# Kernel optimization log

Hardware: AMD Instinct MI355X
Metric: run time of the kernel (lower is better)

Reference implementation:

```python
import jax, jax.numpy as jnp
import numpy as np

NW, NT = 200000, 100000
DW, DT = 128, 64
HID, HEADS, OUT = 64, 2, 2
HC = HID * HEADS  # 128
E = 500000
NEG_SLOPE = 0.2


def setup_inputs() -> dict:
    key = jax.random.key(0)
    ks = iter(jax.random.split(key, 40))

    def nrm(shape, scale):
        return jax.random.normal(next(ks), shape, dtype=jnp.float32) * scale

    inp = {
        "x_wallet": nrm((NW, DW), 1.0),
        "x_token": nrm((NT, DT), 1.0),
        # per-node-type input projections Linear(in, hidden)
        "lin_w_W": nrm((DW, HID), 1.0 / np.sqrt(DW)),
        "lin_w_b": jnp.zeros((HID,), jnp.float32),
        "lin_t_W": nrm((DT, HID), 1.0 / np.sqrt(DT)),
        "lin_t_b": jnp.zeros((HID,), jnp.float32),
        # GAT layer 0: in=HID(64) -> H*C(128), stacked over 3 edge types
        "Wsrc0": nrm((3, HID, HC), 1.0 / np.sqrt(HID)),
        "Wdst0": nrm((3, HID, HC), 1.0 / np.sqrt(HID)),
        "atts0": nrm((3, HEADS, HID), 1.0 / np.sqrt(HID)),
        "attd0": nrm((3, HEADS, HID), 1.0 / np.sqrt(HID)),
        "b0": jnp.zeros((3, HC), jnp.float32),
        # GAT layer 1: in=H*C(128) -> H*C(128)
        "Wsrc1": nrm((3, HC, HC), 1.0 / np.sqrt(HC)),
        "Wdst1": nrm((3, HC, HC), 1.0 / np.sqrt(HC)),
        "atts1": nrm((3, HEADS, HID), 1.0 / np.sqrt(HID)),
        "attd1": nrm((3, HEADS, HID), 1.0 / np.sqrt(HID)),
        "b1": jnp.zeros((3, HC), jnp.float32),
        # classifiers Linear(H*C, out)
        "cls_w_W": nrm((HC, OUT), 1.0 / np.sqrt(HC)),
        "cls_w_b": jnp.zeros((OUT,), jnp.float32),
        "cls_t_W": nrm((HC, OUT), 1.0 / np.sqrt(HC)),
        "cls_t_b": jnp.zeros((OUT,), jnp.float32),
        # edge indices: [2, E] with row0 = src ids, row1 = dst ids
        "e_wt": jnp.stack([jax.random.randint(next(ks), (E,), 0, NW),
                            jax.random.randint(next(ks), (E,), 0, NT)]).astype(jnp.int64),
        "e_tw": jnp.stack([jax.random.randint(next(ks), (E,), 0, NT),
                            jax.random.randint(next(ks), (E,), 0, NW)]).astype(jnp.int64),
        "e_ww": jnp.stack([jax.random.randint(next(ks), (E,), 0, NW),
                            jax.random.randint(next(ks), (E,), 0, NW)]).astype(jnp.int64),
    }
    return inp


def gat_conv(x_src, x_dst, edge, Wsrc, Wdst, att_s, att_d, bias, n_dst):
    # bipartite GATConv: project, per-edge attention, segment softmax over dst, scatter-sum
    hs = (x_src @ Wsrc).reshape(-1, HEADS, HID)  # [Ns,H,C]
    hd = (x_dst @ Wdst).reshape(-1, HEADS, HID)  # [Nd,H,C]
    a_s = jnp.einsum("nhc,hc->nh", hs, att_s)    # [Ns,H]
    a_d = jnp.einsum("nhc,hc->nh", hd, att_d)    # [Nd,H]
    s, d = edge[0], edge[1]
    alpha = jax.nn.leaky_relu(a_s[s] + a_d[d], NEG_SLOPE)  # [E,H]
    m = jax.ops.segment_max(alpha, d, num_segments=n_dst)
    m = jnp.where(jnp.isfinite(m), m, 0.0)  # nodes with no in-edges
    ex = jnp.exp(alpha - m[d])
    den = jax.ops.segment_sum(ex, d, num_segments=n_dst)
    alpha = ex / (den[d] + 1e-16)
    out = jax.ops.segment_sum(alpha[:, :, None] * hs[s], d, num_segments=n_dst)  # [Nd,H,C]
    return out.reshape(n_dst, HC) + bias


def reference(x_wallet, x_token, lin_w_W, lin_w_b, lin_t_W, lin_t_b,
              Wsrc0, Wdst0, atts0, attd0, b0,
              Wsrc1, Wdst1, atts1, attd1, b1,
              cls_w_W, cls_w_b, cls_t_W, cls_t_b,
              e_wt, e_tw, e_ww):
    xw = x_wallet @ lin_w_W + lin_w_b
    xt = x_token @ lin_t_W + lin_t_b
    for Wsrc, Wdst, ats, atd, b in ((Wsrc0, Wdst0, atts0, attd0, b0),
                                     (Wsrc1, Wdst1, atts1, attd1, b1)):
        # edge type 0: wallet->token, 1: token->wallet, 2: wallet->wallet; HeteroConv aggr='sum'
        out_t = gat_conv(xw, xt, e_wt, Wsrc[0], Wdst[0], ats[0], atd[0], b[0], NT)
        out_w = (gat_conv(xt, xw, e_tw, Wsrc[1], Wdst[1], ats[1], atd[1], b[1], NW)
                 + gat_conv(xw, xw, e_ww, Wsrc[2], Wdst[2], ats[2], atd[2], b[2], NW))
        xw = jax.nn.elu(out_w)
        xt = jax.nn.elu(out_t)
    logits_w = xw @ cls_w_W + cls_w_b  # [NW,2]
    logits_t = xt @ cls_t_W + cls_t_b  # [NT,2]
    return jnp.concatenate([logits_w, logits_t], axis=0)  # [NW+NT,2]
```

## Files before the change

### kernel.cpp

```cpp
#include <hip/hip_runtime.h>
#include <stdint.h>

typedef unsigned short ushort_t;
typedef short s8v __attribute__((ext_vector_type(8)));
typedef float f4v __attribute__((ext_vector_type(4)));

#define NW 200000
#define NT 100000
#define EE 500000
#define NSEG (NT + NW + NW)

constexpr int HGRID = 1536;
constexpr int FGRID = 1536;
constexpr int AWG   = (NW + 255) / 256;
constexpr int ATG   = (NT + 255) / 256;
constexpr int TGRID = NT / 4;
constexpr int WGRID = NW / 4;

__device__ __forceinline__ float b2f(unsigned short u){
  union { unsigned int i; float f; } v; v.i = ((unsigned int)u) << 16; return v.f;
}
__device__ __forceinline__ unsigned short f2b(float f){
  unsigned int x = __float_as_uint(f);
  unsigned int r = x + 0x7fffu + ((x >> 16) & 1u);
  return (unsigned short)(r >> 16);
}
__device__ __forceinline__ float ldf(const void* p, long idx, int fm){
  return fm ? ((const float*)p)[idx] : b2f(((const ushort_t*)p)[idx]);
}

__global__ void detect_kern(const int* ewt, const int* etw, const int* eww,
                            const unsigned* xw_words, int* mode){
  if (threadIdx.x == 0 && blockIdx.x == 0){
    unsigned o = 0;
    for (int i = 0; i < 64; ++i)
      o |= (unsigned)ewt[2 * i + 1] | (unsigned)etw[2 * i + 1] | (unsigned)eww[2 * i + 1];
    mode[0] = (o == 0) ? 1 : 0;
    int viol = 0;
    for (int i = 0; i < 256; ++i){
      unsigned s = xw_words[i] & 0xffffu;
      unsigned e = (s >> 7) & 0xffu;
      if (!(s == 0u || s == 0x8000u || (e >= 90u && e <= 140u))) viol++;
    }
    mode[1] = (viol > 8) ? 1 : 0;
  }
}

struct TDesc { const void* src; ushort_t* dst; long ebase; int K; int N; };
struct TDesc8 { TDesc d[8]; };
__device__ __forceinline__ void transpose_body(const TDesc8& td, int fm, int b){
  int mi = b >> 6;
  TDesc t = td.d[mi];
  int e = ((b & 63) << 8) + threadIdx.x;
  if (e < t.K * t.N){
    int k = e / t.N, n = e - k * t.N;
    t.dst[n * t.K + k] = f2b(ldf(t.src, t.ebase + e, fm));
  }
}

__device__ __forceinline__ void uprep_body(const void* Wsrc0, const void* Wdst0, const void* atts0,
    const void* attd0, const void* Wsrc1, const void* Wdst1, const void* atts1, const void* attd1,
    float* Uw0, float* Ut0, float* Uw1, float* Ut1, int fm, int id){
  if (id >= (64 + 128) * 12) return;
  int layer = (id >= 64 * 12);
  int rem = layer ? id - 64 * 12 : id;
  int K = layer ? 128 : 64;
  int k = rem / 12, j = rem % 12;
  const void* Ws = layer ? Wsrc1 : Wsrc0;
  const void* Wd = layer ? Wdst1 : Wdst0;
  const void* As = layer ? atts1 : atts0;
  const void* Ad = layer ? attd1 : attd0;
  int t, h; bool src;
  if (j < 8){ const int tt[8] = {0,0,2,2,1,1,2,2}; t = tt[j]; h = j & 1; src = (j < 4); }
  else { int jj = j - 8; t = (jj < 2) ? 1 : 0; h = jj & 1; src = (jj < 2); }
  const void* W = src ? Ws : Wd;
  const void* A = src ? As : Ad;
  float acc = 0.f;
  for (int c = 0; c < 64; ++c)
    acc += ldf(W, (long)(t * K + k) * 128 + h * 64 + c, fm) * ldf(A, t * 128 + h * 64 + c, fm);
  if (j < 8) (layer ? Uw1 : Uw0)[k * 8 + j] = acc;
  else       (layer ? Ut1 : Ut0)[k * 4 + (j - 8)] = acc;
}

__device__ __forceinline__ void hist_loop(const int* ewt, const int* etw, const int* eww,
    int md, int* deg, int b, int nb){
  int t0 = b * 256 + (int)threadIdx.x;
  int step = nb * 256;
  for (int i = t0; i < 3 * EE; i += step){
    int t = i / EE, e = i - t * EE;
    const int* ep = (t == 0) ? ewt : (t == 1) ? etw : eww;
    int d = md ? ep[2 * (EE + e)] : ep[EE + e];
    int base = (t == 0) ? 0 : (t == 1) ? NT : NT + NW;
    atomicAdd(&deg[base + d], 1);
  }
}

__device__ __forceinline__ void fill_loop(const int* ewt, const int* etw, const int* eww,
    int md, int* cursor, int* adj, int b, int nb){
  int t0 = b * 256 + (int)threadIdx.x;
  int step = nb * 256;
  for (int i = t0; i < 3 * EE; i += step){
    int t = i / EE, e = i - t * EE;
    const int* ep = (t == 0) ? ewt : (t == 1) ? etw : eww;
    int s = md ? ep[2 * e] : ep[e];
    int d = md ? ep[2 * (EE + e)] : ep[EE + e];
    int base = (t == 0) ? 0 : (t == 1) ? NT : NT + NW;
    int pos = atomicAdd(&cursor[base + d], 1);
    adj[pos] = s;
  }
}

__global__ __launch_bounds__(512) void scan1(const int* deg, int* excl, int* sums){
  __shared__ int pair[512];
  int t = threadIdx.x;
  int base = blockIdx.x * 1024;
  int i0 = base + 2 * t;
  int a = (i0 < NSEG) ? deg[i0] : 0;
  int b = (i0 + 1 < NSEG) ? deg[i0 + 1] : 0;
  int ps = a + b;
  pair[t] = ps;
  __syncthreads();
  for (int off = 1; off < 512; off <<= 1){
    int v = (t >= off) ? pair[t - off] : 0;
    __syncthreads();
    if (t >= off) pair[t] += v;
    __syncthreads();
  }
  int epair = pair[t] - ps;
  if (i0 < NSEG) excl[i0] = epair;
  if (i0 + 1 < NSEG) excl[i0 + 1] = epair + a;
  if (t == 511) sums[blockIdx.x] = pair[511];
}

__global__ __launch_bounds__(512) void scan2(int* sums, int nch){
  __shared__ int s[512];
  int t = threadIdx.x;
  int orig = (t < nch) ? sums[t] : 0;
  s[t] = orig;
  __syncthreads();
  for (int off = 1; off < 512; off <<= 1){
    int v = (t >= off) ? s[t - off] : 0;
    __syncthreads();
    if (t >= off) s[t] += v;
    __syncthreads();
  }
  if (t < nch) sums[t] = s[t] - orig;
}

__global__ void scan3(int* rowptr, int* cursor, const int* sums){
  int i = blockIdx.x * 256 + threadIdx.x;
  if (i < NSEG){
    int v = rowptr[i] + sums[i >> 10];
    rowptr[i] = v; cursor[i] = v;
  }
  if (i == 0) rowptr[NSEG] = 3 * EE;
}

template<int K, int NC, int RS, bool BIAS, bool EXTA>
__device__ __forceinline__ void gemm_body(const void* __restrict__ A, const ushort_t* __restrict__ Bt,
    const void* __restrict__ bias, ushort_t* __restrict__ C, int M, int fm, int nchunk,
    int bid, int gstr){
  constexpr int CT = NC / 16, KK = K / 32;
  int tid = threadIdx.x, lane = tid & 63, wave = tid >> 6;
  int rl = lane & 15, kq = (lane >> 4) * 8;
  s8v bfrag[CT][KK];
#pragma unroll
  for (int ct = 0; ct < CT; ++ct)
#pragma unroll
    for (int kk = 0; kk < KK; ++kk)
      bfrag[ct][kk] = *(const s8v*)(Bt + (long)(ct * 16 + rl) * K + kk * 32 + kq);
  float biasv[CT];
  if (BIAS){
#pragma unroll
    for (int ct = 0; ct < CT; ++ct) biasv[ct] = ldf(bias, ct * 16 + rl, fm);
  }
  for (int chunk = bid; chunk < nchunk; chunk += gstr){
    long m0 = (long)chunk * 128 + wave * 32;
    f4v acc[2][CT];
#pragma unroll
    for (int rt = 0; rt < 2; ++rt)
#pragma unroll
      for (int ct = 0; ct < CT; ++ct) acc[rt][ct] = (f4v){0.f, 0.f, 0.f, 0.f};
#pragma unroll
    for (int rt = 0; rt < 2; ++rt){
      long row = m0 + rt * 16 + rl;
      bool ok = row < (long)M;
#pragma unroll
      for (int kk = 0; kk < KK; ++kk){
        s8v a = (s8v){0,0,0,0,0,0,0,0};
        if (ok){
          long e = row * K + kk * 32 + kq;
          if (EXTA && fm){
            const float* p = (const float*)A + e;
            uint4 lo = *(const uint4*)p;
            uint4 hi = *(const uint4*)(p + 4);
            union { s8v v; unsigned u[4]; } t;
            t.u[0] = (unsigned)f2b(__uint_as_float(lo.x)) | ((unsigned)f2b(__uint_as_float(lo.y)) << 16);
            t.u[1] = (unsigned)f2b(__uint_as_float(lo.z)) | ((unsigned)f2b(__uint_as_float(lo.w)) << 16);
            t.u[2] = (unsigned)f2b(__uint_as_float(hi.x)) | ((unsigned)f2b(__uint_as_float(hi.y)) << 16);
            t.u[3] = (unsigned)f2b(__uint_as_float(hi.z)) | ((unsigned)f2b(__uint_as_float(hi.w)) << 16);
            a = t.v;
          } else {
            a = *(const s8v*)((const ushort_t*)A + e);
          }
        }
#pragma unroll
        for (int ct = 0; ct < CT; ++ct)
          acc[rt][ct] = __builtin_amdgcn_mfma_f32_16x16x32_bf16(a, bfrag[ct][kk], acc[rt][ct], 0, 0, 0);
      }
    }
#pragma unroll
    for (int rt = 0; rt < 2; ++rt){
      long rbase = (long)chunk * 128 + wave * 32 + rt * 16 + (lane >> 4) * 4;
#pragma unroll
      for (int ct = 0; ct < CT; ++ct){
#pragma unroll
        for (int r = 0; r < 4; ++r){
          long gm = rbase + r;
          if (gm < (long)M){
            float v = acc[rt][ct][r];
            if (BIAS) v += biasv[ct];
            C[gm * RS + ct * 16 + rl] = f2b(v);
          }
        }
      }
    }
  }
}

template<int K, bool WAL>
__device__ __forceinline__ void a_body(const ushort_t* __restrict__ x, const float* __restrict__ U,
    float* __restrict__ dpq, float* __restrict__ spqA, float* __restrict__ spqB, int N, int n){
  constexpr int NCOL = WAL ? 8 : 4;
  if (n >= N) return;
  float acc[NCOL];
#pragma unroll
  for (int j = 0; j < NCOL; ++j) acc[j] = 0.f;
  const ushort_t* xr = x + (long)n * K;
#pragma unroll
  for (int k8 = 0; k8 < K / 8; ++k8){
    uint4 v = *(const uint4*)(xr + k8 * 8);
    unsigned uu[4] = {v.x, v.y, v.z, v.w};
#pragma unroll
    for (int i = 0; i < 4; ++i){
      float f0 = b2f((unsigned short)(uu[i] & 0xffffu));
      float f1 = b2f((unsigned short)(uu[i] >> 16));
      const float* Ur = U + (k8 * 8 + i * 2) * NCOL;
#pragma unroll
      for (int j = 0; j < NCOL; ++j) acc[j] += f0 * Ur[j] + f1 * Ur[NCOL + j];
    }
  }
  if (WAL){
    f4v tA = {__expf(acc[0]), __expf(0.2f * acc[0]), __expf(acc[1]), __expf(0.2f * acc[1])};
    *(f4v*)(spqA + (long)n * 4) = tA;
    f4v tB = {__expf(acc[2]), __expf(0.2f * acc[2]), __expf(acc[3]), __expf(0.2f * acc[3])};
    *(f4v*)(spqB + (long)n * 4) = tB;
    f4v d1 = {__expf(acc[4]), __expf(0.2f * acc[4]), __expf(acc[5]), __expf(0.2f * acc[5])};
    f4v d2 = {__expf(acc[6]), __expf(0.2f * acc[6]), __expf(acc[7]), __expf(0.2f * acc[7])};
    *(f4v*)(dpq + (long)n * 8) = d1;
    *(f4v*)(dpq + (long)n * 8 + 4) = d2;
  } else {
    f4v tA = {__expf(acc[0]), __expf(0.2f * acc[0]), __expf(acc[1]), __expf(0.2f * acc[1])};
    *(f4v*)(spqA + (long)n * 4) = tA;
    f4v d0 = {__expf(acc[2]), __expf(0.2f * acc[2]), __expf(acc[3]), __expf(0.2f * acc[3])};
    *(f4v*)(dpq + (long)n * 4) = d0;
  }
}

__device__ __forceinline__ void round_load(const int* __restrict__ adj, int j, int cnt,
    const ushort_t* __restrict__ hs, const float* __restrict__ spq, int c0, int hh,
    float2 (&pq)[8], unsigned (&h)[8]){
#pragma unroll
  for (int i = 0; i < 8; ++i){
    if (i < cnt){
      int s = adj[j + i];
      pq[i] = *(const float2*)(spq + s * 4 + hh * 2);
      h[i] = *(const unsigned*)(hs + (long)s * 128 + c0);
    }
  }
}

__device__ __forceinline__ void round_acc(int cnt, float pd, float qd,
    const float2 (&pq)[8], const unsigned (&h)[8], float& n0, float& n1, float& den){
#pragma unroll
  for (int i = 0; i < 8; ++i){
    if (i < cnt){
      float t = pq[i].x * pd, u = pq[i].y * qd;
      float w = t > 1.f ? t : u;
      den += w;
      n0 += w * b2f((unsigned short)(h[i] & 0xffffu));
      n1 += w * b2f((unsigned short)(h[i] >> 16));
    }
  }
}

__device__ __forceinline__ void classify_store(float o0, float o1, const void* W, const void* b,
    int lane, long g, void* dout, int fm){
  float w00 = ldf(W, 4 * lane + 0, fm), w01 = ldf(W, 4 * lane + 1, fm);
  float w10 = ldf(W, 4 * lane + 2, fm), w11 = ldf(W, 4 * lane + 3, fm);
  float p0 = o0 * w00 + o1 * w10;
  float p1 = o0 * w01 + o1 * w11;
#pragma unroll
  for (int off = 32; off > 0; off >>= 1){ p0 += __shfl_xor(p0, off, 64); p1 += __shfl_xor(p1, off, 64); }
  if (lane == 0){
    float r0 = p0 + ldf(b, 0, fm);
    float r1 = p1 + ldf(b, 1, fm);
    if (fm){ ((float*)dout)[g * 2] = r0; ((float*)dout)[g * 2 + 1] = r1; }
    else { ((ushort_t*)dout)[g * 2] = f2b(r0); ((ushort_t*)dout)[g * 2 + 1] = f2b(r1); }
  }
}

template<bool FINAL>
__device__ __forceinline__ void agg_tok_body(const int* __restrict__ rowptr, const int* __restrict__ adj,
    const float* __restrict__ atd, const float* __restrict__ spq0, const ushort_t* __restrict__ hs0,
    const void* __restrict__ bsrc, ushort_t* __restrict__ xt_out,
    const void* __restrict__ clsWt, const void* __restrict__ clsbt,
    void* __restrict__ dout, int fm, int db){
  int wv = __builtin_amdgcn_readfirstlane(threadIdx.x >> 6);
  int lane = threadIdx.x & 63;
  int hh = lane >> 5, c0 = lane << 1;
  int d = db * 4 + wv;
  float2 dq = *(const float2*)(atd + (long)d * 4 + hh * 2);
  int beg = rowptr[d], end = rowptr[d + 1];
  float n0 = 0.f, n1 = 0.f, den = 0.f;
  for (int j = beg; j < end; j += 8){
    int cnt = min(end - j, 8);
    float2 pq[8]; unsigned h[8];
    round_load(adj, j, cnt, hs0, spq0, c0, hh, pq, h);
    round_acc(cnt, dq.x, dq.y, pq, h, n0, n1, den);
  }
  float inv = 1.f / (den + 1e-16f);
  float o0 = n0 * inv + ldf(bsrc, c0, fm);
  float o1 = n1 * inv + ldf(bsrc, c0 + 1, fm);
  o0 = o0 > 0.f ? o0 : __expf(o0) - 1.f;
  o1 = o1 > 0.f ? o1 : __expf(o1) - 1.f;
  if (!FINAL){
    unsigned pack = (unsigned)f2b(o0) | ((unsigned)f2b(o1) << 16);
    *(unsigned*)(xt_out + (long)d * 128 + c0) = pack;
  } else {
    classify_store(o0, o1, clsWt, clsbt, lane, (long)NW + d, dout, fm);
  }
}

template<bool FINAL>
__global__ __launch_bounds__(256) void agg_wal(const int* __restrict__ rowptr, const int* __restrict__ adj,
    const float* __restrict__ awd, const float* __restrict__ spq1, const float* __restrict__ spq2,
    const ushort_t* __restrict__ hs1, const ushort_t* __restrict__ hs2,
    const void* __restrict__ bsrc, ushort_t* __restrict__ xw_out,
    const void* __restrict__ clsWw, const void* __restrict__ clsbw,
    void* __restrict__ dout, const int* __restrict__ mode){
  int fm = mode[1];
  int wv = __builtin_amdgcn_readfirstlane(threadIdx.x >> 6);
  int lane = threadIdx.x & 63;
  int hh = lane >> 5, c0 = lane << 1;
  int d = blockIdx.x * 4 + wv;
  float2 dq1 = *(const float2*)(awd + (long)d * 8 + hh * 2);
  float2 dq2 = *(const float2*)(awd + (long)d * 8 + 4 + hh * 2);
  int s1 = NT + d, s2 = NT + NW + d;
  int b1 = rowptr[s1], e1 = rowptr[s1 + 1];
  int b2 = rowptr[s2], e2 = rowptr[s2 + 1];
  int c1 = min(e1 - b1, 8), c2 = min(e2 - b2, 8);
  float n10 = 0.f, n11 = 0.f, den1 = 0.f;
  float n20 = 0.f, n21 = 0.f, den2 = 0.f;
  {
    float2 pq1[8], pq2[8]; unsigned h1[8], h2[8];
    if (c1 > 0) round_load(adj, b1, c1, hs1, spq1, c0, hh, pq1, h1);
    if (c2 > 0) round_load(adj, b2, c2, hs2, spq2, c0, hh, pq2, h2);
    if (c1 > 0) round_acc(c1, dq1.x, dq1.y, pq1, h1, n10, n11, den1);
    if (c2 > 0) round_acc(c2, dq2.x, dq2.y, pq2, h2, n20, n21, den2);
  }
  for (int j = b1 + 8; j < e1; j += 8){
    int cnt = min(e1 - j, 8);
    float2 pq[8]; unsigned h[8];
    round_load(adj, j, cnt, hs1, spq1, c0, hh, pq, h);
    round_acc(cnt, dq1.x, dq1.y, pq, h, n10, n11, den1);
  }
  for (int j = b2 + 8; j < e2; j += 8){
    int cnt = min(e2 - j, 8);
    float2 pq[8]; unsigned h[8];
    round_load(adj, j, cnt, hs2, spq2, c0, hh, pq, h);
    round_acc(cnt, dq2.x, dq2.y, pq, h, n20, n21, den2);
  }
  float i1v = 1.f / (den1 + 1e-16f), i2v = 1.f / (den2 + 1e-16f);
  float o0 = n10 * i1v + n20 * i2v + ldf(bsrc, 128 + c0, fm)     + ldf(bsrc, 256 + c0, fm);
  float o1 = n11 * i1v + n21 * i2v + ldf(bsrc, 128 + c0 + 1, fm) + ldf(bsrc, 256 + c0 + 1, fm);
  o0 = o0 > 0.f ? o0 : __expf(o0) - 1.f;
  o1 = o1 > 0.f ? o1 : __expf(o1) - 1.f;
  if (!FINAL){
    unsigned pack = (unsigned)f2b(o0) | ((unsigned)f2b(o1) << 16);
    *(unsigned*)(xw_out + (long)d * 128 + c0) = pack;
  } else {
    classify_store(o0, o1, clsWw, clsbw, lane, (long)d, dout, fm);
  }
}


__global__ __launch_bounds__(256) void k_tu(TDesc8 td,
    const void* Wsrc0, const void* Wdst0, const void* atts0, const void* attd0,
    const void* Wsrc1, const void* Wdst1, const void* atts1, const void* attd1,
    float* Uw0, float* Ut0, float* Uw1, float* Ut1, const int* mode){
  int b = blockIdx.x, fm = mode[1];
  if (b < 512){ transpose_body(td, fm, b); return; }
  uprep_body(Wsrc0, Wdst0, atts0, attd0, Wsrc1, Wdst1, atts1, attd1,
             Uw0, Ut0, Uw1, Ut1, fm, (b - 512) * 256 + (int)threadIdx.x);
}

__global__ __launch_bounds__(256, 2) void k_pre(
    const void* xw_in, const ushort_t* BtLw, const void* lwb, ushort_t* xw0,
    const void* xt_in, const ushort_t* BtLt, const void* ltb, ushort_t* xt0,
    const int* ewt, const int* etw, const int* eww, int* deg,
    const int* mode, int ncW, int ncT){
  int b = blockIdx.x;
  if (b < 512){ gemm_body<128, 64, 64, true, true>(xw_in, BtLw, lwb, xw0, NW, mode[1], ncW, b, 512); return; }
  b -= 512;
  if (b < 256){ gemm_body<64, 64, 64, true, true>(xt_in, BtLt, ltb, xt0, NT, mode[1], ncT, b, 256); return; }
  b -= 256;
  hist_loop(ewt, etw, eww, mode[0], deg, b, HGRID);
}

__global__ __launch_bounds__(256, 2) void k_fill(
    const ushort_t* xw0, const ushort_t* xt0, const ushort_t* BtS0w, ushort_t* hs0,
    const float* Uw0, const float* Ut0, float* awd, float* atd,
    float* spq0, float* spq1, float* spq2,
    const int* ewt, const int* etw, const int* eww, int* cursor, int* adj,
    const int* mode, int ncW){
  int b = blockIdx.x;
  if (b < 512){ gemm_body<64, 128, 128, false, false>(xw0, BtS0w, nullptr, hs0, NW, 0, ncW, b, 512); return; }
  b -= 512;
  if (b < FGRID){ fill_loop(ewt, etw, eww, mode[0], cursor, adj, b, FGRID); return; }
  b -= FGRID;
  if (b < AWG){ a_body<64, true>(xw0, Uw0, awd, spq0, spq2, NW, b * 256 + (int)threadIdx.x); return; }
  b -= AWG;
  a_body<64, false>(xt0, Ut0, atd, spq1, nullptr, NT, b * 256 + (int)threadIdx.x);
}

__global__ __launch_bounds__(256, 2) void k_tok0(
    const ushort_t* xt0, const ushort_t* xw0, const ushort_t* BtS0t, const ushort_t* BtS0w2,
    ushort_t* hs1, ushort_t* hs2,
    const int* rowptr, const int* adj, const float* atd, const float* spq0,
    const ushort_t* hs0, const void* b0, ushort_t* xtB,
    const int* mode, int ncT, int ncW){
  int b = blockIdx.x;
  if (b < 256){ gemm_body<64, 128, 128, false, false>(xt0, BtS0t, nullptr, hs1, NT, 0, ncT, b, 256); return; }
  b -= 256;
  if (b < 384){ gemm_body<64, 128, 128, false, false>(xw0, BtS0w2, nullptr, hs2, NW, 0, ncW, b, 384); return; }
  b -= 384;
  agg_tok_body<false>(rowptr, adj, atd, spq0, hs0, b0, xtB, nullptr, nullptr, nullptr, mode[1], b);
}

__global__ __launch_bounds__(256, 2) void k_mid1(
    const ushort_t* xwB, const ushort_t* xtB, const ushort_t* BtS1w, ushort_t* hs0,
    const float* Uw1, const float* Ut1, float* awd, float* atd,
    float* spq0, float* spq1, float* spq2, const int* mode, int ncW){
  int b = blockIdx.x;
  if (b < 512){ gemm_body<128, 128, 128, false, false>(xwB, BtS1w, nullptr, hs0, NW, 0, ncW, b, 512); return; }
  b -= 512;
  if (b < AWG){ a_body<128, true>(xwB, Uw1, awd, spq0, spq2, NW, b * 256 + (int)threadIdx.x); return; }
  b -= AWG;
  a_body<128, false>(xtB, Ut1, atd, spq1, nullptr, NT, b * 256 + (int)threadIdx.x);
}

__global__ __launch_bounds__(256, 2) void k_fin1(
    const ushort_t* xtB, const ushort_t* xwB, const ushort_t* BtS1t, const ushort_t* BtS1w2,
    ushort_t* hs1, ushort_t* hs2,
    const int* rowptr, const int* adj, const float* atd, const float* spq0,
    const ushort_t* hs0, const void* b1, const void* clsWt, const void* clsbt,
    void* dout, const int* mode, int ncT, int ncW){
  int b = blockIdx.x;
  if (b < 256){ gemm_body<128, 128, 128, false, false>(xtB, BtS1t, nullptr, hs1, NT, 0, ncT, b, 256); return; }
  b -= 256;
  if (b < 384){ gemm_body<128, 128, 128, false, false>(xwB, BtS1w2, nullptr, hs2, NW, 0, ncW, b, 384); return; }
  b -= 384;
  agg_tok_body<true>(rowptr, adj, atd, spq0, hs0, b1, nullptr, clsWt, clsbt, dout, mode[1], b);
}

extern "C" void kernel_launch(void* const* d_in, const int* in_sizes, int n_in,
                              void* d_out, int out_size, void* d_ws, size_t ws_size,
                              hipStream_t stream){
  const void* x_wallet = d_in[0];
  const void* x_token  = d_in[1];
  const void* lin_w_W  = d_in[2];
  const void* lin_w_b  = d_in[3];
  const void* lin_t_W  = d_in[4];
  const void* lin_t_b  = d_in[5];
  const void* Wsrc0    = d_in[6];
  const void* Wdst0    = d_in[7];
  const void* atts0    = d_in[8];
  const void* attd0    = d_in[9];
  const void* b0       = d_in[10];
  const void* Wsrc1    = d_in[11];
  const void* Wdst1    = d_in[12];
  const void* atts1    = d_in[13];
  const void* attd1    = d_in[14];
  const void* b1       = d_in[15];
  const void* cls_w_W  = d_in[16];
  const void* cls_w_b  = d_in[17];
  const void* cls_t_W  = d_in[18];
  const void* cls_t_b  = d_in[19];
  const int* e_wt = (const int*)d_in[20];
  const int* e_tw = (const int*)d_in[21];
  const int* e_ww = (const int*)d_in[22];

  char* ws = (char*)d_ws;
  size_t off = 0;
  auto alloc = [&](size_t bytes) -> char* {
    char* p = ws + off; off += (bytes + 255) & ~(size_t)255; return p;
  };
  int* rowptr = (int*)alloc((size_t)(NSEG + 1) * 4);
  int* deg    = (int*)alloc((size_t)(NSEG + 1) * 4);
  int* adj    = (int*)alloc((size_t)3 * EE * 4);
  int* sums   = (int*)alloc(512 * 4);
  int* mode   = (int*)alloc(8);
  ushort_t* BtLw = (ushort_t*)alloc(64 * 128 * 2);
  ushort_t* BtLt = (ushort_t*)alloc(64 * 64 * 2);
  ushort_t* BtS0 = (ushort_t*)alloc(3 * 128 * 64 * 2);
  ushort_t* BtS1 = (ushort_t*)alloc(3 * 128 * 128 * 2);
  float* Uw0 = (float*)alloc(64 * 8 * 4);
  float* Ut0 = (float*)alloc(64 * 4 * 4);
  float* Uw1 = (float*)alloc(128 * 8 * 4);
  float* Ut1 = (float*)alloc(128 * 4 * 4);
  float* awd = (float*)alloc((size_t)NW * 8 * 4);
  float* atd = (float*)alloc((size_t)NT * 4 * 4);
  float* spq0 = (float*)alloc((size_t)NW * 4 * 4);
  float* spq1 = (float*)alloc((size_t)NT * 4 * 4);
  float* spq2 = (float*)alloc((size_t)NW * 4 * 4);
  ushort_t* hs0 = (ushort_t*)alloc((size_t)NW * 128 * 2);
  ushort_t* hs1 = (ushort_t*)alloc((size_t)NT * 128 * 2);
  ushort_t* hs2 = (ushort_t*)alloc((size_t)NW * 128 * 2);
  ushort_t* xbuf = (ushort_t*)alloc(((size_t)NW + NT) * 128 * 2);
  ushort_t* xw0 = xbuf;
  ushort_t* xt0 = xbuf + (size_t)NW * 64;
  ushort_t* xwB = xbuf;
  ushort_t* xtB = xbuf + (size_t)NW * 128;
  (void)in_sizes; (void)n_in;

  if (off > ws_size){
    hipMemsetAsync(d_out, 0, (size_t)out_size * 2, stream);
    return;
  }

  hipMemsetAsync(deg, 0, (size_t)NSEG * 4, stream);
  detect_kern<<<1, 64, 0, stream>>>(e_wt, e_tw, e_ww, (const unsigned*)x_wallet, mode);

  TDesc8 td;
  td.d[0] = { lin_w_W, BtLw, 0, 128, 64 };
  td.d[1] = { lin_t_W, BtLt, 0, 64, 64 };
  for (int t = 0; t < 3; ++t){
    td.d[2 + t] = { Wsrc0, BtS0 + t * 128 * 64,  (long)t * 64 * 128,  64,  128 };
    td.d[5 + t] = { Wsrc1, BtS1 + t * 128 * 128, (long)t * 128 * 128, 128, 128 };
  }
  int ncW = (NW + 127) / 128, ncT = (NT + 127) / 128;

  k_tu<<<521, 256, 0, stream>>>(td, Wsrc0, Wdst0, atts0, attd0, Wsrc1, Wdst1, atts1, attd1,
                                Uw0, Ut0, Uw1, Ut1, mode);
  k_pre<<<512 + 256 + HGRID, 256, 0, stream>>>(x_wallet, BtLw, lin_w_b, xw0,
                                               x_token, BtLt, lin_t_b, xt0,
                                               e_wt, e_tw, e_ww, deg, mode, ncW, ncT);
  int nch = (NSEG + 1023) / 1024;
  scan1<<<nch, 512, 0, stream>>>(deg, rowptr, sums);
  scan2<<<1, 512, 0, stream>>>(sums, nch);
  scan3<<<(NSEG + 255) / 256, 256, 0, stream>>>(rowptr, deg, sums);

  k_fill<<<512 + FGRID + AWG + ATG, 256, 0, stream>>>(xw0, xt0, BtS0, hs0,
      Uw0, Ut0, awd, atd, spq0, spq1, spq2, e_wt, e_tw, e_ww, deg, adj, mode, ncW);
  k_tok0<<<256 + 384 + TGRID, 256, 0, stream>>>(xt0, xw0, BtS0 + 128 * 64, BtS0 + 2 * 128 * 64,
      hs1, hs2, rowptr, adj, atd, spq0, hs0, b0, xtB, mode, ncT, ncW);
  agg_wal<false><<<WGRID, 256, 0, stream>>>(rowptr, adj, awd, spq1, spq2, hs1, hs2, b0, xwB,
                                            nullptr, nullptr, nullptr, mode);

  k_mid1<<<512 + AWG + ATG, 256, 0, stream>>>(xwB, xtB, BtS1, hs0,
      Uw1, Ut1, awd, atd, spq0, spq1, spq2, mode, ncW);
  k_fin1<<<256 + 384 + TGRID, 256, 0, stream>>>(xtB, xwB, BtS1 + 128 * 128, BtS1 + 2 * 128 * 128,
      hs1, hs2, rowptr, adj, atd, spq0, hs0, b1, cls_t_W, cls_t_b, d_out, mode, ncT, ncW);
  agg_wal<true><<<WGRID, 256, 0, stream>>>(rowptr, adj, awd, spq1, spq2, hs1, hs2, b1, nullptr,
                                           cls_w_W, cls_w_b, d_out, mode);
}
```

Measured before the change: 906.8 us.

## Regroup GEMMs into one fused launch and split token aggregation into own kernel

All three source-projection GEMMs for each layer now run in a single fused launch alongside edge fill and attention-score work. Token aggregation becomes its own standalone kernel without the occupancy-2 launch bound. Previously it shared a launch with two GEMMs. The aim is to give the aggregation its own register and occupancy budget and to pack the GEMM work more evenly. The cost is that the GEMMs no longer overlap with the token gather.

```diff
diff --git a/kernel.cpp b/kernel.cpp
--- a/kernel.cpp
+++ b/kernel.cpp
@@ -311,15 +311,16 @@
 }
 
 template<bool FINAL>
-__device__ __forceinline__ void agg_tok_body(const int* __restrict__ rowptr, const int* __restrict__ adj,
+__global__ __launch_bounds__(256) void agg_tok(const int* __restrict__ rowptr, const int* __restrict__ adj,
     const float* __restrict__ atd, const float* __restrict__ spq0, const ushort_t* __restrict__ hs0,
     const void* __restrict__ bsrc, ushort_t* __restrict__ xt_out,
     const void* __restrict__ clsWt, const void* __restrict__ clsbt,
-    void* __restrict__ dout, int fm, int db){
+    void* __restrict__ dout, const int* __restrict__ mode){
+  int fm = mode[1];
   int wv = __builtin_amdgcn_readfirstlane(threadIdx.x >> 6);
   int lane = threadIdx.x & 63;
   int hh = lane >> 5, c0 = lane << 1;
-  int d = db * 4 + wv;
+  int d = blockIdx.x * 4 + wv;
   float2 dq = *(const float2*)(atd + (long)d * 4 + hh * 2);
   int beg = rowptr[d], end = rowptr[d + 1];
   float n0 = 0.f, n1 = 0.f, den = 0.f;
@@ -418,15 +419,21 @@
   hist_loop(ewt, etw, eww, mode[0], deg, b, HGRID);
 }
 
-__global__ __launch_bounds__(256, 2) void k_fill(
-    const ushort_t* xw0, const ushort_t* xt0, const ushort_t* BtS0w, ushort_t* hs0,
+__global__ __launch_bounds__(256, 2) void k_gemms0(
+    const ushort_t* xw0, const ushort_t* xt0,
+    const ushort_t* BtS0w, const ushort_t* BtS0t, const ushort_t* BtS0w2,
+    ushort_t* hs0, ushort_t* hs1, ushort_t* hs2,
     const float* Uw0, const float* Ut0, float* awd, float* atd,
     float* spq0, float* spq1, float* spq2,
     const int* ewt, const int* etw, const int* eww, int* cursor, int* adj,
-    const int* mode, int ncW){
+    const int* mode, int ncW, int ncT){
   int b = blockIdx.x;
   if (b < 512){ gemm_body<64, 128, 128, false, false>(xw0, BtS0w, nullptr, hs0, NW, 0, ncW, b, 512); return; }
   b -= 512;
+  if (b < 256){ gemm_body<64, 128, 128, false, false>(xt0, BtS0t, nullptr, hs1, NT, 0, ncT, b, 256); return; }
+  b -= 256;
+  if (b < 384){ gemm_body<64, 128, 128, false, false>(xw0, BtS0w2, nullptr, hs2, NW, 0, ncW, b, 384); return; }
+  b -= 384;
   if (b < FGRID){ fill_loop(ewt, etw, eww, mode[0], cursor, adj, b, FGRID); return; }
   b -= FGRID;
   if (b < AWG){ a_body<64, true>(xw0, Uw0, awd, spq0, spq2, NW, b * 256 + (int)threadIdx.x); return; }
@@ -434,44 +441,22 @@
   a_body<64, false>(xt0, Ut0, atd, spq1, nullptr, NT, b * 256 + (int)threadIdx.x);
 }
 
-__global__ __launch_bounds__(256, 2) void k_tok0(
-    const ushort_t* xt0, const ushort_t* xw0, const ushort_t* BtS0t, const ushort_t* BtS0w2,
-    ushort_t* hs1, ushort_t* hs2,
-    const int* rowptr, const int* adj, const float* atd, const float* spq0,
-    const ushort_t* hs0, const void* b0, ushort_t* xtB,
-    const int* mode, int ncT, int ncW){
-  int b = blockIdx.x;
-  if (b < 256){ gemm_body<64, 128, 128, false, false>(xt0, BtS0t, nullptr, hs1, NT, 0, ncT, b, 256); return; }
-  b -= 256;
-  if (b < 384){ gemm_body<64, 128, 128, false, false>(xw0, BtS0w2, nullptr, hs2, NW, 0, ncW, b, 384); return; }
-  b -= 384;
-  agg_tok_body<false>(rowptr, adj, atd, spq0, hs0, b0, xtB, nullptr, nullptr, nullptr, mode[1], b);
-}
-
-__global__ __launch_bounds__(256, 2) void k_mid1(
-    const ushort_t* xwB, const ushort_t* xtB, const ushort_t* BtS1w, ushort_t* hs0,
+__global__ __launch_bounds__(256, 2) void k_gemms1(
+    const ushort_t* xwB, const ushort_t* xtB,
+    const ushort_t* BtS1w, const ushort_t* BtS1t, const ushort_t* BtS1w2,
+    ushort_t* hs0, ushort_t* hs1, ushort_t* hs2,
     const float* Uw1, const float* Ut1, float* awd, float* atd,
-    float* spq0, float* spq1, float* spq2, const int* mode, int ncW){
+    float* spq0, float* spq1, float* spq2, const int* mode, int ncW, int ncT){
   int b = blockIdx.x;
   if (b < 512){ gemm_body<128, 128, 128, false, false>(xwB, BtS1w, nullptr, hs0, NW, 0, ncW, b, 512); return; }
   b -= 512;
-  if (b < AWG){ a_body<128, true>(xwB, Uw1, awd, spq0, spq2, NW, b * 256 + (int)threadIdx.x); return; }
-  b -= AWG;
-  a_body<128, false>(xtB, Ut1, atd, spq1, nullptr, NT, b * 256 + (int)threadIdx.x);
-}
-
-__global__ __launch_bounds__(256, 2) void k_fin1(
-    const ushort_t* xtB, const ushort_t* xwB, const ushort_t* BtS1t, const ushort_t* BtS1w2,
-    ushort_t* hs1, ushort_t* hs2,
-    const int* rowptr, const int* adj, const float* atd, const float* spq0,
-    const ushort_t* hs0, const void* b1, const void* clsWt, const void* clsbt,
-    void* dout, const int* mode, int ncT, int ncW){
-  int b = blockIdx.x;
   if (b < 256){ gemm_body<128, 128, 128, false, false>(xtB, BtS1t, nullptr, hs1, NT, 0, ncT, b, 256); return; }
   b -= 256;
   if (b < 384){ gemm_body<128, 128, 128, false, false>(xwB, BtS1w2, nullptr, hs2, NW, 0, ncW, b, 384); return; }
   b -= 384;
-  agg_tok_body<true>(rowptr, adj, atd, spq0, hs0, b1, nullptr, clsWt, clsbt, dout, mode[1], b);
+  if (b < AWG){ a_body<128, true>(xwB, Uw1, awd, spq0, spq2, NW, b * 256 + (int)threadIdx.x); return; }
+  b -= AWG;
+  a_body<128, false>(xtB, Ut1, atd, spq1, nullptr, NT, b * 256 + (int)threadIdx.x);
 }
 
 extern "C" void kernel_launch(void* const* d_in, const int* in_sizes, int n_in,
@@ -561,17 +546,19 @@
   scan2<<<1, 512, 0, stream>>>(sums, nch);
   scan3<<<(NSEG + 255) / 256, 256, 0, stream>>>(rowptr, deg, sums);
 
-  k_fill<<<512 + FGRID + AWG + ATG, 256, 0, stream>>>(xw0, xt0, BtS0, hs0,
-      Uw0, Ut0, awd, atd, spq0, spq1, spq2, e_wt, e_tw, e_ww, deg, adj, mode, ncW);
-  k_tok0<<<256 + 384 + TGRID, 256, 0, stream>>>(xt0, xw0, BtS0 + 128 * 64, BtS0 + 2 * 128 * 64,
-      hs1, hs2, rowptr, adj, atd, spq0, hs0, b0, xtB, mode, ncT, ncW);
+  k_gemms0<<<512 + 256 + 384 + FGRID + AWG + ATG, 256, 0, stream>>>(xw0, xt0,
+      BtS0, BtS0 + 128 * 64, BtS0 + 2 * 128 * 64, hs0, hs1, hs2,
+      Uw0, Ut0, awd, atd, spq0, spq1, spq2, e_wt, e_tw, e_ww, deg, adj, mode, ncW, ncT);
+  agg_tok<false><<<TGRID, 256, 0, stream>>>(rowptr, adj, atd, spq0, hs0, b0, xtB,
+                                            nullptr, nullptr, nullptr, mode);
   agg_wal<false><<<WGRID, 256, 0, stream>>>(rowptr, adj, awd, spq1, spq2, hs1, hs2, b0, xwB,
                                             nullptr, nullptr, nullptr, mode);
 
-  k_mid1<<<512 + AWG + ATG, 256, 0, stream>>>(xwB, xtB, BtS1, hs0,
-      Uw1, Ut1, awd, atd, spq0, spq1, spq2, mode, ncW);
-  k_fin1<<<256 + 384 + TGRID, 256, 0, stream>>>(xtB, xwB, BtS1 + 128 * 128, BtS1 + 2 * 128 * 128,
-      hs1, hs2, rowptr, adj, atd, spq0, hs0, b1, cls_t_W, cls_t_b, d_out, mode, ncT, ncW);
+  k_gemms1<<<512 + 256 + 384 + AWG + ATG, 256, 0, stream>>>(xwB, xtB,
+      BtS1, BtS1 + 128 * 128, BtS1 + 2 * 128 * 128, hs0, hs1, hs2,
+      Uw1, Ut1, awd, atd, spq0, spq1, spq2, mode, ncW, ncT);
+  agg_tok<true><<<TGRID, 256, 0, stream>>>(rowptr, adj, atd, spq0, hs0, b1, nullptr,
+                                           cls_t_W, cls_t_b, d_out, mode);
   agg_wal<true><<<WGRID, 256, 0, stream>>>(rowptr, adj, awd, spq1, spq2, hs1, hs2, b1, nullptr,
                                            cls_w_W, cls_w_b, d_out, mode);
 }
```

After: 806.2 us. 11.1% less time.
